# Kernel tuning notes

Hardware: AMD Instinct MI355X
Metric: run time of the kernel (lower is better)

Reference implementation:

```python
import jax, jax.numpy as jnp
import numpy as np

X_DIM, Z_DIM, N_HEIGHT = 256, 256, 32
EPS = 1e-5  # BatchNorm1d eps

def _bn(x, g, b):
    # BatchNorm1d in training mode: batch statistics over the point axis
    m = x.mean(0)
    v = x.var(0)
    return (x - m) * jax.lax.rsqrt(v + EPS) * g + b

def setup_inputs() -> dict:
    key = jax.random.key(0)
    ks = jax.random.split(key, 16)
    B, N, F = 2, 120000, 3
    inp = {
        'pt_fea': jax.random.normal(ks[0], (B, N, F), jnp.float32),
        'grid_ind': jax.random.randint(ks[1], (B, N, 2), 0, 256, dtype=jnp.int32).astype(jnp.int64),
        'occupancy': (jax.random.uniform(ks[2], (B, 1, X_DIM, N_HEIGHT, Z_DIM)) < 0.1).astype(jnp.float32),
    }
    dims = [(3, 64), (64, 128), (128, 256), (256, 512)]
    for i, (di, do) in enumerate(dims):
        inp[f'W{i+1}'] = jax.random.normal(ks[3 + i], (di, do), jnp.float32) * 0.02
        inp[f'b{i+1}'] = jnp.zeros((do,), jnp.float32)
    for i, d in enumerate([3, 64, 128, 256]):
        inp[f'g{i}'] = jnp.ones((d,), jnp.float32)
        inp[f'be{i}'] = jnp.zeros((d,), jnp.float32)
    inp['Wc'] = jax.random.normal(ks[10], (512, 32), jnp.float32) * 0.02
    inp['bc'] = jnp.zeros((32,), jnp.float32)
    return inp

def reference(pt_fea, occupancy, W1, b1, W2, b2, W3, b3, W4, b4,
              g0, be0, g1, be1, g2, be2, g3, be3, Wc, bc, grid_ind):
    B, N, F = pt_fea.shape
    feats = pt_fea.reshape(B * N, F)                          # cat over batch
    # PointNet per-point MLP: BN -> (Linear -> BN -> ReLU) x3 -> Linear
    h = _bn(feats, g0, be0)
    h = jax.nn.relu(_bn(h @ W1 + b1, g1, be1))
    h = jax.nn.relu(_bn(h @ W2 + b2, g2, be2))
    h = jax.nn.relu(_bn(h @ W3 + b3, g3, be3))
    h = h @ W4 + b4                                           # [B*N, 512]

    # linear segment id per (batch, x, z) cell; equivalent to unique+scatter_max
    gi = grid_ind.reshape(B * N, 2).astype(jnp.int32)
    batch_idx = jnp.repeat(jnp.arange(B, dtype=jnp.int32), N)
    seg = batch_idx * (X_DIM * Z_DIM) + gi[:, 0] * Z_DIM + gi[:, 1]
    n_cells = B * X_DIM * Z_DIM

    pooled = jax.ops.segment_max(h, seg, num_segments=n_cells)          # [cells, 512]
    cnt = jax.ops.segment_sum(jnp.ones((B * N,), h.dtype), seg, num_segments=n_cells)
    occ_mask = (cnt > 0)[:, None]
    pooled = jnp.where(occ_mask, pooled, 0.0)                           # kill -inf empties

    # feature compression on occupied cells only; empty cells stay exactly 0
    comp = jax.nn.relu(pooled @ Wc + bc)
    comp = jnp.where(occ_mask, comp, 0.0)                               # [cells, 32]

    bev = comp.reshape(B, X_DIM, Z_DIM, -1).transpose(0, 3, 1, 2)       # [B, 32, X, Z]
    # MaxPool2d(k=3, stride=1, pad=1); -inf padding matches torch's implicit -inf pad
    bev = jax.lax.reduce_window(bev, -jnp.inf, jax.lax.max,
                                (1, 1, 3, 3), (1, 1, 1, 1), 'SAME')

    occu = occupancy[:, 0].transpose(0, 2, 1, 3)                        # [B, H, X, Z]
    out = jnp.concatenate([occu, bev], axis=1)                          # [B, H+32, X, Z]
    return out
```

## Files before the change

kernel.cpp:

```cpp
#include <hip/hip_runtime.h>
#include <hip/hip_bf16.h>

#define EPSN 1e-5f

typedef __bf16 bf16x8 __attribute__((ext_vector_type(8)));
typedef float f32x4 __attribute__((ext_vector_type(4)));

__device__ __forceinline__ unsigned encf(float f) {
  unsigned u = __float_as_uint(f);
  return (u & 0x80000000u) ? ~u : (u | 0x80000000u);
}
__device__ __forceinline__ float decf(unsigned u) {
  return (u & 0x80000000u) ? __uint_as_float(u ^ 0x80000000u) : __uint_as_float(~u);
}

__global__ __launch_bounds__(256) void stats_feats(const float* __restrict__ pt, int n,
                                                   float* __restrict__ sums) {
  float a0 = 0, a1 = 0, a2 = 0, q0 = 0, q1 = 0, q2 = 0;
  for (int p = blockIdx.x * 256 + threadIdx.x; p < n; p += gridDim.x * 256) {
    float v0 = pt[3 * p], v1 = pt[3 * p + 1], v2 = pt[3 * p + 2];
    a0 += v0; a1 += v1; a2 += v2;
    q0 += v0 * v0; q1 += v1 * v1; q2 += v2 * v2;
  }
  __shared__ float red[4][6];
  float vals[6] = {a0, a1, a2, q0, q1, q2};
  int lane = threadIdx.x & 63, wv = threadIdx.x >> 6;
#pragma unroll
  for (int k = 0; k < 6; k++) {
    float v = vals[k];
#pragma unroll
    for (int o = 32; o; o >>= 1) v += __shfl_down(v, o, 64);
    if (lane == 0) red[wv][k] = v;
  }
  __syncthreads();
  if (threadIdx.x < 6) {
    float v = red[0][threadIdx.x] + red[1][threadIdx.x] + red[2][threadIdx.x] + red[3][threadIdx.x];
    atomicAdd(&sums[threadIdx.x], v);
  }
}

__global__ void bn_prep(const float* __restrict__ sums, int C, float invN,
                        const float* __restrict__ g, const float* __restrict__ be,
                        float* __restrict__ sc, float* __restrict__ sh) {
  int c = threadIdx.x;
  if (c < C) {
    float m = sums[c] * invN;
    float v = fmaxf(sums[C + c] * invN - m * m, 0.f);
    float s = g[c] * rsqrtf(v + EPSN);
    sc[c] = s;
    sh[c] = be[c] - m * s;
  }
}

__global__ __launch_bounds__(256) void wconv(const float* __restrict__ W,
                                             __hip_bfloat16* __restrict__ Wt, int K, int C) {
  int idx = blockIdx.x * 256 + threadIdx.x;
  if (idx >= K * C) return;
  int k = idx / C, c = idx - k * C;
  Wt[(size_t)c * K + k] = __float2bfloat16(W[idx]);
}

__global__ __launch_bounds__(256) void gemm1_stats(const float* __restrict__ pt,
                                                   const float* __restrict__ W,
                                                   const float* __restrict__ bias,
                                                   const float* __restrict__ scsh,
                                                   __hip_bfloat16* __restrict__ Y,
                                                   int n, float* __restrict__ sums) {
  const int c = threadIdx.x & 63;
  const float w0 = W[c], w1 = W[64 + c], w2 = W[128 + c], bb = bias[c];
  const float s0 = scsh[0], s1 = scsh[1], s2 = scsh[2];
  const float h0 = scsh[4], h1 = scsh[5], h2 = scsh[6];
  float s = 0.f, q = 0.f;
  const int total = n * 64;
  for (int idx = blockIdx.x * 256 + threadIdx.x; idx < total; idx += gridDim.x * 256) {
    int p = idx >> 6;
    float x0 = s0 * pt[3 * p]     + h0;
    float x1 = s1 * pt[3 * p + 1] + h1;
    float x2 = s2 * pt[3 * p + 2] + h2;
    float y = bb + x0 * w0 + x1 * w1 + x2 * w2;
    Y[idx] = __float2bfloat16(y);
    s += y; q += y * y;
  }
  __shared__ float sred[4][64], qred[4][64];
  int wv = threadIdx.x >> 6;
  sred[wv][c] = s; qred[wv][c] = q;
  __syncthreads();
  if (threadIdx.x < 64) {
    float S = sred[0][c] + sred[1][c] + sred[2][c] + sred[3][c];
    float Q = qred[0][c] + qred[1][c] + qred[2][c] + qred[3][c];
    atomicAdd(&sums[c], S);
    atomicAdd(&sums[64 + c], Q);
  }
}

template <int K>
__global__ __launch_bounds__(256) void gemm_mfma(
    const __hip_bfloat16* __restrict__ Yin, const __hip_bfloat16* __restrict__ Wt,
    const float* __restrict__ bias, const float* __restrict__ sc, const float* __restrict__ sh,
    __hip_bfloat16* __restrict__ Yout, int C, float* __restrict__ sums, int nrows) {
  constexpr int KS = 64, LDA = 72, LDO = 80;
  __shared__ __align__(16) __hip_bfloat16 hA[128 * LDO];
  __shared__ float sredArr[128], qredArr[128];
  const int t = threadIdx.x;
  const int lane = t & 63, wv = t >> 6;
  const int mh = (wv >> 1) * 64, nh = (wv & 1) * 64;
  const int lm = lane & 15, lq = lane >> 4;
  const int p0 = blockIdx.x * 128;
  const int cb0 = blockIdx.y * 128;

  f32x4 acc[4][4];
#pragma unroll
  for (int i = 0; i < 4; i++)
#pragma unroll
    for (int j = 0; j < 4; j++) acc[i][j] = {0.f, 0.f, 0.f, 0.f};

  for (int k0 = 0; k0 < K; k0 += KS) {
    __syncthreads();
#pragma unroll
    for (int it = 0; it < 4; it++) {
      int idx = it * 256 + t;
      int row = idx >> 3;
      int c8 = (idx & 7) * 8;
      int gp = p0 + row;
      __hip_bfloat16 h8[8];
      if (gp < nrows) {
        uint4 raw = *(const uint4*)(Yin + (size_t)gp * K + k0 + c8);
        const __hip_bfloat16* pr = (const __hip_bfloat16*)&raw;
#pragma unroll
        for (int j = 0; j < 8; j++) {
          float v = sc[k0 + c8 + j] * __bfloat162float(pr[j]) + sh[k0 + c8 + j];
          h8[j] = __float2bfloat16(fmaxf(v, 0.f));
        }
      } else {
#pragma unroll
        for (int j = 0; j < 8; j++) h8[j] = __float2bfloat16(0.f);
      }
      *(uint4*)&hA[row * LDA + c8] = *(const uint4*)h8;
    }
    __syncthreads();
#pragma unroll
    for (int kk = 0; kk < KS; kk += 32) {
      bf16x8 a[4], b[4];
#pragma unroll
      for (int i = 0; i < 4; i++)
        a[i] = *(const bf16x8*)&hA[(mh + i * 16 + lm) * LDA + kk + lq * 8];
#pragma unroll
      for (int j = 0; j < 4; j++)
        b[j] = *(const bf16x8*)(const void*)(Wt + (size_t)(cb0 + nh + j * 16 + lm) * K + k0 + kk + lq * 8);
#pragma unroll
      for (int i = 0; i < 4; i++)
#pragma unroll
        for (int j = 0; j < 4; j++)
          acc[i][j] = __builtin_amdgcn_mfma_f32_16x16x32_bf16(a[i], b[j], acc[i][j], 0, 0, 0);
    }
  }

#pragma unroll
  for (int j = 0; j < 4; j++) {
    float bb = bias[cb0 + nh + j * 16 + lm];
#pragma unroll
    for (int i = 0; i < 4; i++)
#pragma unroll
      for (int r = 0; r < 4; r++) acc[i][j][r] += bb;
  }

  __syncthreads();
  if (t < 128) { sredArr[t] = 0.f; qredArr[t] = 0.f; }
  __syncthreads();

#pragma unroll
  for (int j = 0; j < 4; j++) {
    float s = 0.f, q = 0.f;
#pragma unroll
    for (int i = 0; i < 4; i++)
#pragma unroll
      for (int r = 0; r < 4; r++) {
        int grow = p0 + mh + i * 16 + lq * 4 + r;
        if (grow < nrows) { float v = acc[i][j][r]; s += v; q += v * v; }
      }
    s += __shfl_xor(s, 16); s += __shfl_xor(s, 32);
    q += __shfl_xor(q, 16); q += __shfl_xor(q, 32);
    if (lq == 0) {
      atomicAdd(&sredArr[nh + j * 16 + lm], s);
      atomicAdd(&qredArr[nh + j * 16 + lm], q);
    }
  }

  for (int half = 0; half < 2; half++) {
    __syncthreads();
    if ((wv & 1) == half) {
#pragma unroll
      for (int j = 0; j < 4; j++)
#pragma unroll
        for (int i = 0; i < 4; i++)
#pragma unroll
          for (int r = 0; r < 4; r++)
            hA[(mh + i * 16 + lq * 4 + r) * LDO + j * 16 + lm] = __float2bfloat16(acc[i][j][r]);
    }
    __syncthreads();
    int row = t >> 1, seg = t & 1;
    if (p0 + row < nrows) {
      const uint4* src = (const uint4*)&hA[row * LDO + seg * 32];
      uint4* dst = (uint4*)(Yout + (size_t)(p0 + row) * C + cb0 + half * 64 + seg * 32);
      dst[0] = src[0]; dst[1] = src[1]; dst[2] = src[2]; dst[3] = src[3];
    }
  }

  if (t < 128) {
    atomicAdd(&sums[cb0 + t], sredArr[t]);
    atomicAdd(&sums[C + cb0 + t], qredArr[t]);
  }
}

__global__ __launch_bounds__(256) void hist_kernel(const int* __restrict__ gi, int perB,
                                                   unsigned* __restrict__ hist) {
  int b = blockIdx.y;
  int p = blockIdx.x * 256 + threadIdx.x;
  if (p < perB) {
    int gp = b * perB + p;
    int c = (gi[2 * gp] & 255) * 256 + (gi[2 * gp + 1] & 255);
    atomicAdd(&hist[b * 65536 + c], 1u);
  }
}
__global__ __launch_bounds__(256) void scan1(const unsigned* __restrict__ hist,
                                             unsigned* __restrict__ cursor,
                                             unsigned* __restrict__ bSums) {
  __shared__ unsigned s[256];
  int b = blockIdx.y;
  int t = threadIdx.x, i = b * 65536 + blockIdx.x * 256 + t;
  unsigned v = hist[i]; s[t] = v; __syncthreads();
  for (int off = 1; off < 256; off <<= 1) {
    unsigned x = (t >= off) ? s[t - off] : 0u; __syncthreads();
    s[t] += x; __syncthreads();
  }
  cursor[i] = s[t] - v;
  if (t == 255) bSums[b * 256 + blockIdx.x] = s[255];
}
__global__ void scan2(unsigned* __restrict__ bSums) {
  __shared__ unsigned s[256];
  int t = threadIdx.x, i = blockIdx.x * 256 + t;
  unsigned v = bSums[i]; s[t] = v; __syncthreads();
  for (int off = 1; off < 256; off <<= 1) {
    unsigned x = (t >= off) ? s[t - off] : 0u; __syncthreads();
    s[t] += x; __syncthreads();
  }
  bSums[i] = s[t] - v;
}
__global__ __launch_bounds__(256) void mk_starts(const unsigned* __restrict__ cursor,
                                                 const unsigned* __restrict__ bSums,
                                                 unsigned* __restrict__ starts, int perB) {
  int b = blockIdx.y;
  int i = blockIdx.x * 256 + threadIdx.x;
  starts[b * 65537 + i] = cursor[b * 65536 + i] + bSums[b * 256 + (i >> 8)];
  if (i == 0) starts[b * 65537 + 65536] = (unsigned)perB;
}
__global__ __launch_bounds__(256) void scatter_kernel(const int* __restrict__ gi, int perB,
                                                      unsigned* __restrict__ cursor,
                                                      const unsigned* __restrict__ bSums,
                                                      unsigned* __restrict__ sorted,
                                                      unsigned* __restrict__ cells) {
  int b = blockIdx.y;
  int p = blockIdx.x * 256 + threadIdx.x;
  if (p < perB) {
    int gp = b * perB + p;
    int c = (gi[2 * gp] & 255) * 256 + (gi[2 * gp + 1] & 255);
    unsigned pos = atomicAdd(&cursor[b * 65536 + c], 1u) + bSums[b * 256 + (c >> 8)];
    if (pos < (unsigned)perB) {
      sorted[b * perB + pos] = (unsigned)p;
      cells[b * perB + pos] = (unsigned)c;
    }
  }
}

__global__ __launch_bounds__(256, 2) void pool_compress(
    const __hip_bfloat16* __restrict__ Y3, const __hip_bfloat16* __restrict__ Wt4,
    const float* __restrict__ b4, const float* __restrict__ sc, const float* __restrict__ sh,
    const __hip_bfloat16* __restrict__ WcT, const float* __restrict__ bc,
    const unsigned* __restrict__ sortedIdx, const unsigned* __restrict__ sortedCell,
    const unsigned* __restrict__ startsAll, float* __restrict__ comp, int perB) {
  constexpr int K = 256, KS = 64, LDA = 72, MLW = 132;
  __shared__ __align__(16) __hip_bfloat16 hA[128 * LDA];
  __shared__ __align__(16) unsigned maxLds[64 * MLW];
  __shared__ unsigned char slotRow[256];
  __shared__ int rowIdxLds[256];
  const int t = threadIdx.x;
  const int lane = t & 63, wv = t >> 6;
  const int lm = lane & 15, lq = lane >> 4;
  const int mh = (wv >> 1) * 64, nh = (wv & 1) * 64;
  const int batch = blockIdx.y;
  const unsigned* starts = startsAll + batch * 65537;
  const int c0 = blockIdx.x * 64;
  const int r0 = (int)starts[c0];
  int n = (int)starts[c0 + 64] - r0;
  if (n > 256) n = 256;
  if (n < 0) n = 0;
  const int nrg = (n + 127) >> 7;

  for (int i = t; i < n; i += 256) {
    rowIdxLds[i] = (int)sortedIdx[batch * perB + r0 + i] + batch * perB;
    slotRow[i] = (unsigned char)((sortedCell[batch * perB + r0 + i] - c0) & 63);
  }

  f32x4 accC[2];
  accC[0] = {0.f, 0.f, 0.f, 0.f};
  accC[1] = {0.f, 0.f, 0.f, 0.f};

  for (int cc = 0; cc < 4; cc++) {
    __syncthreads();
    for (int i = t; i < 64 * MLW; i += 256) maxLds[i] = 0u;
    for (int rg = 0; rg < nrg; rg++) {
      const int rbase = rg * 128;
      f32x4 acc[4][4];
#pragma unroll
      for (int i = 0; i < 4; i++)
#pragma unroll
        for (int j = 0; j < 4; j++) acc[i][j] = {0.f, 0.f, 0.f, 0.f};
      for (int k0 = 0; k0 < K; k0 += KS) {
        __syncthreads();
#pragma unroll
        for (int it = 0; it < 4; it++) {
          int idx = it * 256 + t;
          int row = idx >> 3;
          int c8 = (idx & 7) * 8;
          int gr = rbase + row;
          __hip_bfloat16 h8[8];
          if (gr < n) {
            uint4 raw = *(const uint4*)(Y3 + (size_t)rowIdxLds[gr] * K + k0 + c8);
            const __hip_bfloat16* pr = (const __hip_bfloat16*)&raw;
#pragma unroll
            for (int j = 0; j < 8; j++) {
              float v = sc[k0 + c8 + j] * __bfloat162float(pr[j]) + sh[k0 + c8 + j];
              h8[j] = __float2bfloat16(fmaxf(v, 0.f));
            }
          } else {
#pragma unroll
            for (int j = 0; j < 8; j++) h8[j] = __float2bfloat16(0.f);
          }
          *(uint4*)&hA[row * LDA + c8] = *(const uint4*)h8;
        }
        __syncthreads();
#pragma unroll
        for (int kk = 0; kk < KS; kk += 32) {
          bf16x8 a[4], b[4];
#pragma unroll
          for (int i = 0; i < 4; i++)
            a[i] = *(const bf16x8*)&hA[(mh + i * 16 + lm) * LDA + kk + lq * 8];
#pragma unroll
          for (int j = 0; j < 4; j++)
            b[j] = *(const bf16x8*)(const void*)(Wt4 + (size_t)(cc * 128 + nh + j * 16 + lm) * K + k0 + kk + lq * 8);
#pragma unroll
          for (int i = 0; i < 4; i++)
#pragma unroll
            for (int j = 0; j < 4; j++)
              acc[i][j] = __builtin_amdgcn_mfma_f32_16x16x32_bf16(a[i], b[j], acc[i][j], 0, 0, 0);
        }
      }
#pragma unroll
      for (int j = 0; j < 4; j++) {
        int colq = nh + j * 16 + lm;
#pragma unroll
        for (int i = 0; i < 4; i++) {
#pragma unroll
          for (int r = 0; r < 4; r++) {
            int lrow = rbase + mh + i * 16 + lq * 4 + r;
            if (lrow < n)
              atomicMax(&maxLds[(int)slotRow[lrow] * MLW + colq], encf(acc[i][j][r]));
          }
        }
      }
    }
    __syncthreads();
#pragma unroll
    for (int ks = 0; ks < 4; ks++) {
      int koff = ks * 32 + lq * 8;
      uint4 m0 = *(const uint4*)&maxLds[(wv * 16 + lm) * MLW + koff];
      uint4 m1 = *(const uint4*)&maxLds[(wv * 16 + lm) * MLW + koff + 4];
      unsigned mu[8] = {m0.x, m0.y, m0.z, m0.w, m1.x, m1.y, m1.z, m1.w};
      __hip_bfloat16 af[8];
#pragma unroll
      for (int j = 0; j < 8; j++)
        af[j] = __float2bfloat16(decf(mu[j]) + b4[cc * 128 + koff + j]);
      bf16x8 a = *(const bf16x8*)af;
#pragma unroll
      for (int jn = 0; jn < 2; jn++) {
        bf16x8 b = *(const bf16x8*)(const void*)(WcT + (size_t)(jn * 16 + lm) * 512 + cc * 128 + koff);
        accC[jn] = __builtin_amdgcn_mfma_f32_16x16x32_bf16(a, b, accC[jn], 0, 0, 0);
      }
    }
  }
#pragma unroll
  for (int jn = 0; jn < 2; jn++) {
    float bb = bc[jn * 16 + lm];
#pragma unroll
    for (int r = 0; r < 4; r++) {
      int cell = c0 + wv * 16 + lq * 4 + r;
      int occ = starts[cell + 1] > starts[cell];
      float v = occ ? fmaxf(accC[jn][r] + bb, 0.f) : 0.f;
      comp[((size_t)batch * 65536 + cell) * 32 + jn * 16 + lm] = v;
    }
  }
}

__global__ __launch_bounds__(256) void maxpool_write(const float* __restrict__ comp,
                                                     float* __restrict__ out) {
  __shared__ float tile[32][65];
  int bid = blockIdx.x;
  int z0 = (bid & 3) * 64, x = (bid >> 2) & 255, b = bid >> 10;
  int f = threadIdx.x & 31, zs = threadIdx.x >> 5;
  for (int zi = 0; zi < 8; zi++) {
    int z = z0 + zi * 8 + zs;
    float m = -3.402823466e38f;
    for (int dx = -1; dx <= 1; dx++) {
      int xx = x + dx;
      if (xx < 0 || xx > 255) continue;
      for (int dz = -1; dz <= 1; dz++) {
        int zz = z + dz;
        if (zz < 0 || zz > 255) continue;
        m = fmaxf(m, comp[(size_t)((b << 16) + (xx << 8) + zz) * 32 + f]);
      }
    }
    tile[f][zi * 8 + zs] = m;
  }
  __syncthreads();
  int f2 = threadIdx.x >> 3, seg = threadIdx.x & 7;
  float* dst = out + ((size_t)(b * 64 + 32 + f2) * 256 + x) * 256 + z0 + seg * 8;
#pragma unroll
  for (int u = 0; u < 8; u++) dst[u] = tile[f2][seg * 8 + u];
}

__global__ __launch_bounds__(256) void occu_write(const float* __restrict__ occ,
                                                  float* __restrict__ out) {
  int idx = blockIdx.x * 256 + threadIdx.x;
  int z = idx & 255, x = (idx >> 8) & 255, hh = (idx >> 16) & 31, b = idx >> 21;
  out[((size_t)(b * 64 + hh) * 256 + x) * 256 + z] =
      occ[((size_t)((b * 256 + x) * 32 + hh)) * 256 + z];
}

extern "C" void kernel_launch(void* const* d_in, const int* in_sizes, int n_in,
                              void* d_out, int out_size, void* d_ws, size_t ws_size,
                              hipStream_t stream) {
  const float* pt_fea   = (const float*)d_in[0];
  const int*   grid_ind = (const int*)d_in[1];
  const float* occup    = (const float*)d_in[2];
  const float* W1 = (const float*)d_in[3];  const float* b1 = (const float*)d_in[4];
  const float* W2 = (const float*)d_in[5];  const float* b2 = (const float*)d_in[6];
  const float* W3 = (const float*)d_in[7];  const float* b3 = (const float*)d_in[8];
  const float* W4 = (const float*)d_in[9];  const float* b4 = (const float*)d_in[10];
  const float* g0 = (const float*)d_in[11]; const float* be0 = (const float*)d_in[12];
  const float* g1 = (const float*)d_in[13]; const float* be1 = (const float*)d_in[14];
  const float* g2 = (const float*)d_in[15]; const float* be2 = (const float*)d_in[16];
  const float* g3 = (const float*)d_in[17]; const float* be3 = (const float*)d_in[18];
  const float* Wc = (const float*)d_in[19]; const float* bc = (const float*)d_in[20];
  float* out = (float*)d_out;

  const int nPts = in_sizes[0] / 3;
  const int perB = nPts / 2;
  const float invN = 1.f / (float)nPts;

  char* ws = (char*)d_ws;
  float* stats = (float*)ws;
  float* scsh  = (float*)(ws + 4096);
  float* sums0 = stats;        float* sums1 = stats + 16;
  float* sums2 = stats + 160;  float* sums3 = stats + 416;
  float* sc0 = scsh;
  float* sc1 = scsh + 16;   float* sh1 = scsh + 80;
  float* sc2 = scsh + 144;  float* sh2 = scsh + 272;
  float* sc3 = scsh + 400;  float* sh3 = scsh + 656;
  __hip_bfloat16* Wt2 = (__hip_bfloat16*)(ws + 8192);
  __hip_bfloat16* Wt3 = (__hip_bfloat16*)(ws + 24576);
  __hip_bfloat16* Wt4 = (__hip_bfloat16*)(ws + 90112);
  __hip_bfloat16* WcT = (__hip_bfloat16*)(ws + 352256);
  char* S0 = ws + 385024;
  __hip_bfloat16* Y1 = (__hip_bfloat16*)S0;
  __hip_bfloat16* Y2 = (__hip_bfloat16*)(S0 + 30720000ll);
  __hip_bfloat16* Y3 = (__hip_bfloat16*)(S0 + 92160000ll);
  float* comp       = (float*)S0;
  char* sortBase    = S0 + 16777216ll;
  unsigned* hist    = (unsigned*)sortBase;
  unsigned* cursor  = hist + 2 * 65536;
  unsigned* bSums   = cursor + 2 * 65536;
  unsigned* startsA = bSums + 1024;
  unsigned* sorted  = startsA + 131080;
  unsigned* cells   = sorted + 2 * perB;

  hipMemsetAsync(stats, 0, 4096, stream);

  wconv<<<(64 * 128 + 255) / 256, 256, 0, stream>>>(W2, Wt2, 64, 128);
  wconv<<<(128 * 256 + 255) / 256, 256, 0, stream>>>(W3, Wt3, 128, 256);
  wconv<<<(256 * 512 + 255) / 256, 256, 0, stream>>>(W4, Wt4, 256, 512);
  wconv<<<(512 * 32 + 255) / 256, 256, 0, stream>>>(Wc, WcT, 512, 32);

  stats_feats<<<256, 256, 0, stream>>>(pt_fea, nPts, sums0);
  bn_prep<<<1, 256, 0, stream>>>(sums0, 3, invN, g0, be0, sc0, scsh + 4);

  gemm1_stats<<<512, 256, 0, stream>>>(pt_fea, W1, b1, scsh, Y1, nPts, sums1);
  bn_prep<<<1, 256, 0, stream>>>(sums1, 64, invN, g1, be1, sc1, sh1);

  gemm_mfma<64><<<dim3(nPts / 128, 1), 256, 0, stream>>>(Y1, Wt2, b2, sc1, sh1, Y2, 128, sums2, nPts);
  bn_prep<<<1, 256, 0, stream>>>(sums2, 128, invN, g2, be2, sc2, sh2);

  gemm_mfma<128><<<dim3(nPts / 128, 2), 256, 0, stream>>>(Y2, Wt3, b3, sc2, sh2, Y3, 256, sums3, nPts);
  bn_prep<<<1, 256, 0, stream>>>(sums3, 256, invN, g3, be3, sc3, sh3);

  hipMemsetAsync(hist, 0, 2 * 65536 * 4, stream);
  const int pgrid = (perB + 255) / 256;
  hist_kernel<<<dim3(pgrid, 2), 256, 0, stream>>>(grid_ind, perB, hist);
  scan1<<<dim3(256, 2), 256, 0, stream>>>(hist, cursor, bSums);
  scan2<<<2, 256, 0, stream>>>(bSums);
  mk_starts<<<dim3(256, 2), 256, 0, stream>>>(cursor, bSums, startsA, perB);
  scatter_kernel<<<dim3(pgrid, 2), 256, 0, stream>>>(grid_ind, perB, cursor, bSums, sorted, cells);

  pool_compress<<<dim3(1024, 2), 256, 0, stream>>>(
      Y3, Wt4, b4, sc3, sh3, WcT, bc, sorted, cells, startsA, comp, perB);

  maxpool_write<<<2048, 256, 0, stream>>>(comp, out);
  occu_write<<<16384, 256, 0, stream>>>(occup, out);
}
```

Measured before the change: 771.8 us.

## Restructure pool_compress to keep A rows in registers with 512-thread blocks

Rewrites the fused GEMM4+segment-max kernel so each of 8 waves loads its 16 gathered rows straight into registers (applying BN+ReLU on the fly) instead of staging through an LDS tile. When a block has at most 128 points, the A fragments are loaded once and reused across all four 128-column chunks. This removes the repeated gathers and the LDS round trip. Block size doubles to 512 and the max buffer is zeroed during the compress step rather than in a separate pass. The cost is higher register pressure from the 8-fragment A cache and 8 accumulators, plus half the waves sitting idle during the compress MFMA step.

```diff
diff --git a/kernel.cpp b/kernel.cpp
--- a/kernel.cpp
+++ b/kernel.cpp
@@ -272,21 +272,19 @@
   }
 }
 
-__global__ __launch_bounds__(256, 2) void pool_compress(
+__global__ __launch_bounds__(512, 4) void pool_compress(
     const __hip_bfloat16* __restrict__ Y3, const __hip_bfloat16* __restrict__ Wt4,
     const float* __restrict__ b4, const float* __restrict__ sc, const float* __restrict__ sh,
     const __hip_bfloat16* __restrict__ WcT, const float* __restrict__ bc,
     const unsigned* __restrict__ sortedIdx, const unsigned* __restrict__ sortedCell,
     const unsigned* __restrict__ startsAll, float* __restrict__ comp, int perB) {
-  constexpr int K = 256, KS = 64, LDA = 72, MLW = 132;
-  __shared__ __align__(16) __hip_bfloat16 hA[128 * LDA];
+  constexpr int K = 256, MLW = 132;
   __shared__ __align__(16) unsigned maxLds[64 * MLW];
   __shared__ unsigned char slotRow[256];
   __shared__ int rowIdxLds[256];
   const int t = threadIdx.x;
   const int lane = t & 63, wv = t >> 6;
   const int lm = lane & 15, lq = lane >> 4;
-  const int mh = (wv >> 1) * 64, nh = (wv & 1) * 64;
   const int batch = blockIdx.y;
   const unsigned* starts = startsAll + batch * 65537;
   const int c0 = blockIdx.x * 64;
@@ -294,109 +292,120 @@
   int n = (int)starts[c0 + 64] - r0;
   if (n > 256) n = 256;
   if (n < 0) n = 0;
-  const int nrg = (n + 127) >> 7;
-
-  for (int i = t; i < n; i += 256) {
+
+  for (int i = t; i < n; i += 512) {
     rowIdxLds[i] = (int)sortedIdx[batch * perB + r0 + i] + batch * perB;
     slotRow[i] = (unsigned char)((sortedCell[batch * perB + r0 + i] - c0) & 63);
   }
-
+  for (int i = t; i < 64 * MLW; i += 512) maxLds[i] = 0u;
+  __syncthreads();
+
+  const bool fast = (n <= 128);
+  bf16x8 a[8];
   f32x4 accC[2];
   accC[0] = {0.f, 0.f, 0.f, 0.f};
   accC[1] = {0.f, 0.f, 0.f, 0.f};
 
+  auto loadA = [&](int base) {
+    int row = base + wv * 16 + lm;
+    if (row < n) {
+      const __hip_bfloat16* src = Y3 + (size_t)rowIdxLds[row] * K;
+#pragma unroll
+      for (int kk = 0; kk < 8; kk++) {
+        int col = kk * 32 + lq * 8;
+        uint4 raw = *(const uint4*)(src + col);
+        const __hip_bfloat16* pr = (const __hip_bfloat16*)&raw;
+        float4 sca = *(const float4*)(sc + col);
+        float4 scb = *(const float4*)(sc + col + 4);
+        float4 sha = *(const float4*)(sh + col);
+        float4 shb = *(const float4*)(sh + col + 4);
+        float scv[8] = {sca.x, sca.y, sca.z, sca.w, scb.x, scb.y, scb.z, scb.w};
+        float shv[8] = {sha.x, sha.y, sha.z, sha.w, shb.x, shb.y, shb.z, shb.w};
+        __hip_bfloat16 h8[8];
+#pragma unroll
+        for (int e = 0; e < 8; e++) {
+          float v = fmaf(scv[e], __bfloat162float(pr[e]), shv[e]);
+          h8[e] = __float2bfloat16(fmaxf(v, 0.f));
+        }
+        a[kk] = *(const bf16x8*)h8;
+      }
+    } else {
+      __hip_bfloat16 z8[8];
+#pragma unroll
+      for (int e = 0; e < 8; e++) z8[e] = __float2bfloat16(0.f);
+#pragma unroll
+      for (int kk = 0; kk < 8; kk++) a[kk] = *(const bf16x8*)z8;
+    }
+  };
+
+  auto mfmaAtomic = [&](int cc, int base) {
+    f32x4 acc[8];
+#pragma unroll
+    for (int j = 0; j < 8; j++) acc[j] = {0.f, 0.f, 0.f, 0.f};
+#pragma unroll
+    for (int kk = 0; kk < 8; kk++) {
+#pragma unroll
+      for (int j = 0; j < 8; j++) {
+        bf16x8 b = *(const bf16x8*)(const void*)(Wt4 + (size_t)(cc * 128 + j * 16 + lm) * K + kk * 32 + lq * 8);
+        acc[j] = __builtin_amdgcn_mfma_f32_16x16x32_bf16(a[kk], b, acc[j], 0, 0, 0);
+      }
+    }
+#pragma unroll
+    for (int j = 0; j < 8; j++) {
+#pragma unroll
+      for (int r = 0; r < 4; r++) {
+        int lrow = base + wv * 16 + lq * 4 + r;
+        if (lrow < n)
+          atomicMax(&maxLds[(int)slotRow[lrow] * MLW + j * 16 + lm], encf(acc[j][r]));
+      }
+    }
+  };
+
   for (int cc = 0; cc < 4; cc++) {
+    if (!fast || cc == 0) loadA(0);
+    mfmaAtomic(cc, 0);
+    if (!fast) {
+      loadA(128);
+      mfmaAtomic(cc, 128);
+    }
     __syncthreads();
-    for (int i = t; i < 64 * MLW; i += 256) maxLds[i] = 0u;
-    for (int rg = 0; rg < nrg; rg++) {
-      const int rbase = rg * 128;
-      f32x4 acc[4][4];
-#pragma unroll
-      for (int i = 0; i < 4; i++)
-#pragma unroll
-        for (int j = 0; j < 4; j++) acc[i][j] = {0.f, 0.f, 0.f, 0.f};
-      for (int k0 = 0; k0 < K; k0 += KS) {
-        __syncthreads();
-#pragma unroll
-        for (int it = 0; it < 4; it++) {
-          int idx = it * 256 + t;
-          int row = idx >> 3;
-          int c8 = (idx & 7) * 8;
-          int gr = rbase + row;
-          __hip_bfloat16 h8[8];
-          if (gr < n) {
-            uint4 raw = *(const uint4*)(Y3 + (size_t)rowIdxLds[gr] * K + k0 + c8);
-            const __hip_bfloat16* pr = (const __hip_bfloat16*)&raw;
-#pragma unroll
-            for (int j = 0; j < 8; j++) {
-              float v = sc[k0 + c8 + j] * __bfloat162float(pr[j]) + sh[k0 + c8 + j];
-              h8[j] = __float2bfloat16(fmaxf(v, 0.f));
-            }
-          } else {
-#pragma unroll
-            for (int j = 0; j < 8; j++) h8[j] = __float2bfloat16(0.f);
-          }
-          *(uint4*)&hA[row * LDA + c8] = *(const uint4*)h8;
+    if (wv < 4) {
+#pragma unroll
+      for (int ks = 0; ks < 4; ks++) {
+        int koff = ks * 32 + lq * 8;
+        unsigned* mp = &maxLds[(wv * 16 + lm) * MLW + koff];
+        uint4 m0 = *(const uint4*)mp;
+        uint4 m1 = *(const uint4*)(mp + 4);
+        unsigned mu[8] = {m0.x, m0.y, m0.z, m0.w, m1.x, m1.y, m1.z, m1.w};
+        __hip_bfloat16 af[8];
+#pragma unroll
+        for (int j = 0; j < 8; j++)
+          af[j] = __float2bfloat16(decf(mu[j]) + b4[cc * 128 + koff + j]);
+        bf16x8 aa = *(const bf16x8*)af;
+        const uint4 z4 = {0u, 0u, 0u, 0u};
+        *(uint4*)mp = z4;
+        *(uint4*)(mp + 4) = z4;
+#pragma unroll
+        for (int jn = 0; jn < 2; jn++) {
+          bf16x8 b = *(const bf16x8*)(const void*)(WcT + (size_t)(jn * 16 + lm) * 512 + cc * 128 + koff);
+          accC[jn] = __builtin_amdgcn_mfma_f32_16x16x32_bf16(aa, b, accC[jn], 0, 0, 0);
         }
-        __syncthreads();
-#pragma unroll
-        for (int kk = 0; kk < KS; kk += 32) {
-          bf16x8 a[4], b[4];
-#pragma unroll
-          for (int i = 0; i < 4; i++)
-            a[i] = *(const bf16x8*)&hA[(mh + i * 16 + lm) * LDA + kk + lq * 8];
-#pragma unroll
-          for (int j = 0; j < 4; j++)
-            b[j] = *(const bf16x8*)(const void*)(Wt4 + (size_t)(cc * 128 + nh + j * 16 + lm) * K + k0 + kk + lq * 8);
-#pragma unroll
-          for (int i = 0; i < 4; i++)
-#pragma unroll
-            for (int j = 0; j < 4; j++)
-              acc[i][j] = __builtin_amdgcn_mfma_f32_16x16x32_bf16(a[i], b[j], acc[i][j], 0, 0, 0);
-        }
-      }
-#pragma unroll
-      for (int j = 0; j < 4; j++) {
-        int colq = nh + j * 16 + lm;
-#pragma unroll
-        for (int i = 0; i < 4; i++) {
-#pragma unroll
-          for (int r = 0; r < 4; r++) {
-            int lrow = rbase + mh + i * 16 + lq * 4 + r;
-            if (lrow < n)
-              atomicMax(&maxLds[(int)slotRow[lrow] * MLW + colq], encf(acc[i][j][r]));
-          }
-        }
       }
     }
     __syncthreads();
-#pragma unroll
-    for (int ks = 0; ks < 4; ks++) {
-      int koff = ks * 32 + lq * 8;
-      uint4 m0 = *(const uint4*)&maxLds[(wv * 16 + lm) * MLW + koff];
-      uint4 m1 = *(const uint4*)&maxLds[(wv * 16 + lm) * MLW + koff + 4];
-      unsigned mu[8] = {m0.x, m0.y, m0.z, m0.w, m1.x, m1.y, m1.z, m1.w};
-      __hip_bfloat16 af[8];
-#pragma unroll
-      for (int j = 0; j < 8; j++)
-        af[j] = __float2bfloat16(decf(mu[j]) + b4[cc * 128 + koff + j]);
-      bf16x8 a = *(const bf16x8*)af;
-#pragma unroll
-      for (int jn = 0; jn < 2; jn++) {
-        bf16x8 b = *(const bf16x8*)(const void*)(WcT + (size_t)(jn * 16 + lm) * 512 + cc * 128 + koff);
-        accC[jn] = __builtin_amdgcn_mfma_f32_16x16x32_bf16(a, b, accC[jn], 0, 0, 0);
-      }
-    }
-  }
-#pragma unroll
-  for (int jn = 0; jn < 2; jn++) {
-    float bb = bc[jn * 16 + lm];
-#pragma unroll
-    for (int r = 0; r < 4; r++) {
-      int cell = c0 + wv * 16 + lq * 4 + r;
-      int occ = starts[cell + 1] > starts[cell];
-      float v = occ ? fmaxf(accC[jn][r] + bb, 0.f) : 0.f;
-      comp[((size_t)batch * 65536 + cell) * 32 + jn * 16 + lm] = v;
+  }
+
+  if (wv < 4) {
+#pragma unroll
+    for (int jn = 0; jn < 2; jn++) {
+      float bb = bc[jn * 16 + lm];
+#pragma unroll
+      for (int r = 0; r < 4; r++) {
+        int cell = c0 + wv * 16 + lq * 4 + r;
+        int occ = starts[cell + 1] > starts[cell];
+        float v = occ ? fmaxf(accC[jn][r] + bb, 0.f) : 0.f;
+        comp[((size_t)batch * 65536 + cell) * 32 + jn * 16 + lm] = v;
+      }
     }
   }
 }
@@ -510,7 +519,7 @@
   mk_starts<<<dim3(256, 2), 256, 0, stream>>>(cursor, bSums, startsA, perB);
   scatter_kernel<<<dim3(pgrid, 2), 256, 0, stream>>>(grid_ind, perB, cursor, bSums, sorted, cells);
 
-  pool_compress<<<dim3(1024, 2), 256, 0, stream>>>(
+  pool_compress<<<dim3(1024, 2), 512, 0, stream>>>(
       Y3, Wt4, b4, sc3, sh3, WcT, bc, sorted, cells, startsA, comp, perB);
 
   maxpool_write<<<2048, 256, 0, stream>>>(comp, out);
```

Measured after the change: 1.276 ms. +65.3%, slower.

## Restructure pool_compress to 32 cells per block with full 512-column tile

Applied to the files above, without the earlier changes.

The pooling kernel now handles 32 cells per block instead of 64. Each wave computes 128 of the 512 output columns for 64-row groups, so the loop over four column chunks is gone. Each gathered Y3 row now goes through the BN+ReLU transform and LDS staging once, instead of once per column chunk, which removes 4x redundant gather and compute. In exchange, the max buffer grows to 32x516 words, there are 32 accumulators per thread (register pressure), the grid is twice as large, and only two waves do the compression GEMM.

```diff
diff --git a/kernel.cpp b/kernel.cpp
--- a/kernel.cpp
+++ b/kernel.cpp
@@ -278,125 +278,123 @@
     const __hip_bfloat16* __restrict__ WcT, const float* __restrict__ bc,
     const unsigned* __restrict__ sortedIdx, const unsigned* __restrict__ sortedCell,
     const unsigned* __restrict__ startsAll, float* __restrict__ comp, int perB) {
-  constexpr int K = 256, KS = 64, LDA = 72, MLW = 132;
-  __shared__ __align__(16) __hip_bfloat16 hA[128 * LDA];
-  __shared__ __align__(16) unsigned maxLds[64 * MLW];
+  constexpr int K = 256, KS = 64, LDA = 72, MLW = 516;
+  __shared__ __align__(16) __hip_bfloat16 hA[64 * LDA];
+  __shared__ __align__(16) unsigned maxLds[32 * MLW];
   __shared__ unsigned char slotRow[256];
   __shared__ int rowIdxLds[256];
   const int t = threadIdx.x;
   const int lane = t & 63, wv = t >> 6;
   const int lm = lane & 15, lq = lane >> 4;
-  const int mh = (wv >> 1) * 64, nh = (wv & 1) * 64;
   const int batch = blockIdx.y;
   const unsigned* starts = startsAll + batch * 65537;
-  const int c0 = blockIdx.x * 64;
+  const int c0 = blockIdx.x * 32;
   const int r0 = (int)starts[c0];
-  int n = (int)starts[c0 + 64] - r0;
+  int n = (int)starts[c0 + 32] - r0;
   if (n > 256) n = 256;
   if (n < 0) n = 0;
-  const int nrg = (n + 127) >> 7;
+  const int nrg = (n + 63) >> 6;
 
   for (int i = t; i < n; i += 256) {
     rowIdxLds[i] = (int)sortedIdx[batch * perB + r0 + i] + batch * perB;
-    slotRow[i] = (unsigned char)((sortedCell[batch * perB + r0 + i] - c0) & 63);
-  }
-
-  f32x4 accC[2];
-  accC[0] = {0.f, 0.f, 0.f, 0.f};
-  accC[1] = {0.f, 0.f, 0.f, 0.f};
-
-  for (int cc = 0; cc < 4; cc++) {
-    __syncthreads();
-    for (int i = t; i < 64 * MLW; i += 256) maxLds[i] = 0u;
-    for (int rg = 0; rg < nrg; rg++) {
-      const int rbase = rg * 128;
-      f32x4 acc[4][4];
-#pragma unroll
-      for (int i = 0; i < 4; i++)
-#pragma unroll
-        for (int j = 0; j < 4; j++) acc[i][j] = {0.f, 0.f, 0.f, 0.f};
-      for (int k0 = 0; k0 < K; k0 += KS) {
-        __syncthreads();
-#pragma unroll
-        for (int it = 0; it < 4; it++) {
-          int idx = it * 256 + t;
-          int row = idx >> 3;
-          int c8 = (idx & 7) * 8;
-          int gr = rbase + row;
-          __hip_bfloat16 h8[8];
-          if (gr < n) {
-            uint4 raw = *(const uint4*)(Y3 + (size_t)rowIdxLds[gr] * K + k0 + c8);
-            const __hip_bfloat16* pr = (const __hip_bfloat16*)&raw;
-#pragma unroll
-            for (int j = 0; j < 8; j++) {
-              float v = sc[k0 + c8 + j] * __bfloat162float(pr[j]) + sh[k0 + c8 + j];
-              h8[j] = __float2bfloat16(fmaxf(v, 0.f));
-            }
-          } else {
-#pragma unroll
-            for (int j = 0; j < 8; j++) h8[j] = __float2bfloat16(0.f);
+    slotRow[i] = (unsigned char)((sortedCell[batch * perB + r0 + i] - c0) & 31);
+  }
+  for (int i = t; i < 32 * MLW; i += 256) maxLds[i] = 0u;
+
+  for (int rg = 0; rg < nrg; rg++) {
+    const int rbase = rg * 64;
+    f32x4 acc[4][8];
+#pragma unroll
+    for (int i = 0; i < 4; i++)
+#pragma unroll
+      for (int j = 0; j < 8; j++) acc[i][j] = {0.f, 0.f, 0.f, 0.f};
+    for (int k0 = 0; k0 < K; k0 += KS) {
+      __syncthreads();
+#pragma unroll
+      for (int it = 0; it < 2; it++) {
+        int idx = it * 256 + t;
+        int row = idx >> 3;
+        int c8 = (idx & 7) * 8;
+        int gr = rbase + row;
+        __hip_bfloat16 h8[8];
+        if (gr < n) {
+          uint4 raw = *(const uint4*)(Y3 + (size_t)rowIdxLds[gr] * K + k0 + c8);
+          const __hip_bfloat16* pr = (const __hip_bfloat16*)&raw;
+#pragma unroll
+          for (int j = 0; j < 8; j++) {
+            float v = sc[k0 + c8 + j] * __bfloat162float(pr[j]) + sh[k0 + c8 + j];
+            h8[j] = __float2bfloat16(fmaxf(v, 0.f));
           }
-          *(uint4*)&hA[row * LDA + c8] = *(const uint4*)h8;
+        } else {
+#pragma unroll
+          for (int j = 0; j < 8; j++) h8[j] = __float2bfloat16(0.f);
         }
-        __syncthreads();
-#pragma unroll
-        for (int kk = 0; kk < KS; kk += 32) {
-          bf16x8 a[4], b[4];
+        *(uint4*)&hA[row * LDA + c8] = *(const uint4*)h8;
+      }
+      __syncthreads();
+#pragma unroll
+      for (int kk = 0; kk < KS; kk += 32) {
+        bf16x8 a[4];
+#pragma unroll
+        for (int i = 0; i < 4; i++)
+          a[i] = *(const bf16x8*)&hA[(i * 16 + lm) * LDA + kk + lq * 8];
+#pragma unroll
+        for (int j = 0; j < 8; j++) {
+          bf16x8 b = *(const bf16x8*)(const void*)(Wt4 + (size_t)(wv * 128 + j * 16 + lm) * K + k0 + kk + lq * 8);
 #pragma unroll
           for (int i = 0; i < 4; i++)
-            a[i] = *(const bf16x8*)&hA[(mh + i * 16 + lm) * LDA + kk + lq * 8];
-#pragma unroll
-          for (int j = 0; j < 4; j++)
-            b[j] = *(const bf16x8*)(const void*)(Wt4 + (size_t)(cc * 128 + nh + j * 16 + lm) * K + k0 + kk + lq * 8);
-#pragma unroll
-          for (int i = 0; i < 4; i++)
-#pragma unroll
-            for (int j = 0; j < 4; j++)
-              acc[i][j] = __builtin_amdgcn_mfma_f32_16x16x32_bf16(a[i], b[j], acc[i][j], 0, 0, 0);
+            acc[i][j] = __builtin_amdgcn_mfma_f32_16x16x32_bf16(a[i], b, acc[i][j], 0, 0, 0);
         }
       }
-#pragma unroll
-      for (int j = 0; j < 4; j++) {
-        int colq = nh + j * 16 + lm;
-#pragma unroll
-        for (int i = 0; i < 4; i++) {
-#pragma unroll
-          for (int r = 0; r < 4; r++) {
-            int lrow = rbase + mh + i * 16 + lq * 4 + r;
-            if (lrow < n)
-              atomicMax(&maxLds[(int)slotRow[lrow] * MLW + colq], encf(acc[i][j][r]));
-          }
+    }
+#pragma unroll
+    for (int j = 0; j < 8; j++) {
+      int col = wv * 128 + j * 16 + lm;
+#pragma unroll
+      for (int i = 0; i < 4; i++) {
+#pragma unroll
+        for (int r = 0; r < 4; r++) {
+          int lrow = rbase + i * 16 + lq * 4 + r;
+          if (lrow < n)
+            atomicMax(&maxLds[(int)slotRow[lrow] * MLW + col], encf(acc[i][j][r]));
         }
       }
     }
-    __syncthreads();
-#pragma unroll
-    for (int ks = 0; ks < 4; ks++) {
+  }
+  __syncthreads();
+
+  if (wv < 2) {
+    f32x4 accC[2];
+    accC[0] = {0.f, 0.f, 0.f, 0.f};
+    accC[1] = {0.f, 0.f, 0.f, 0.f};
+#pragma unroll
+    for (int ks = 0; ks < 16; ks++) {
       int koff = ks * 32 + lq * 8;
-      uint4 m0 = *(const uint4*)&maxLds[(wv * 16 + lm) * MLW + koff];
-      uint4 m1 = *(const uint4*)&maxLds[(wv * 16 + lm) * MLW + koff + 4];
+      const unsigned* mp = &maxLds[(wv * 16 + lm) * MLW + koff];
+      uint4 m0 = *(const uint4*)mp;
+      uint4 m1 = *(const uint4*)(mp + 4);
       unsigned mu[8] = {m0.x, m0.y, m0.z, m0.w, m1.x, m1.y, m1.z, m1.w};
       __hip_bfloat16 af[8];
 #pragma unroll
       for (int j = 0; j < 8; j++)
-        af[j] = __float2bfloat16(decf(mu[j]) + b4[cc * 128 + koff + j]);
-      bf16x8 a = *(const bf16x8*)af;
+        af[j] = __float2bfloat16(decf(mu[j]) + b4[koff + j]);
+      bf16x8 aa = *(const bf16x8*)af;
 #pragma unroll
       for (int jn = 0; jn < 2; jn++) {
-        bf16x8 b = *(const bf16x8*)(const void*)(WcT + (size_t)(jn * 16 + lm) * 512 + cc * 128 + koff);
-        accC[jn] = __builtin_amdgcn_mfma_f32_16x16x32_bf16(a, b, accC[jn], 0, 0, 0);
-      }
-    }
-  }
-#pragma unroll
-  for (int jn = 0; jn < 2; jn++) {
-    float bb = bc[jn * 16 + lm];
-#pragma unroll
-    for (int r = 0; r < 4; r++) {
-      int cell = c0 + wv * 16 + lq * 4 + r;
-      int occ = starts[cell + 1] > starts[cell];
-      float v = occ ? fmaxf(accC[jn][r] + bb, 0.f) : 0.f;
-      comp[((size_t)batch * 65536 + cell) * 32 + jn * 16 + lm] = v;
+        bf16x8 b = *(const bf16x8*)(const void*)(WcT + (size_t)(jn * 16 + lm) * 512 + koff);
+        accC[jn] = __builtin_amdgcn_mfma_f32_16x16x32_bf16(aa, b, accC[jn], 0, 0, 0);
+      }
+    }
+#pragma unroll
+    for (int jn = 0; jn < 2; jn++) {
+      float bb = bc[jn * 16 + lm];
+#pragma unroll
+      for (int r = 0; r < 4; r++) {
+        int cell = c0 + wv * 16 + lq * 4 + r;
+        int occ = starts[cell + 1] > starts[cell];
+        float v = occ ? fmaxf(accC[jn][r] + bb, 0.f) : 0.f;
+        comp[((size_t)batch * 65536 + cell) * 32 + jn * 16 + lm] = v;
+      }
     }
   }
 }
@@ -510,7 +508,7 @@
   mk_starts<<<dim3(256, 2), 256, 0, stream>>>(cursor, bSums, startsA, perB);
   scatter_kernel<<<dim3(pgrid, 2), 256, 0, stream>>>(grid_ind, perB, cursor, bSums, sorted, cells);
 
-  pool_compress<<<dim3(1024, 2), 256, 0, stream>>>(
+  pool_compress<<<dim3(2048, 2), 256, 0, stream>>>(
       Y3, Wt4, b4, sc3, sh3, WcT, bc, sorted, cells, startsA, comp, perB);
 
   maxpool_write<<<2048, 256, 0, stream>>>(comp, out);
```

Result: faster. 728.8 us (-5.6%).
